# Kernel optimization log

Measured on AMD Instinct MI355X. Metric: run time of the kernel, lower is better.

Reference implementation:

```python
import jax, jax.numpy as jnp
import numpy as np

B, CIN, COUT, K, H, W = 16, 256, 256, 3, 64, 64
COND = 512


def setup_inputs() -> dict:
    key = jax.random.key(0)
    ks = jax.random.split(key, 10)
    X = jax.random.normal(ks[0], (B, CIN, H, W), dtype=jnp.float32)
    cond_v = jax.random.normal(ks[1], (B, COND), dtype=jnp.float32)
    # conv weight [O, I, kh, kw]
    conv_w = jax.random.normal(ks[2], (COUT, CIN, K, K), dtype=jnp.float32) / np.sqrt(CIN * K * K)
    w0 = jax.random.normal(ks[3], (COND, COND), dtype=jnp.float32) / np.sqrt(COND)
    b0 = jnp.zeros((COND,), dtype=jnp.float32)
    w1 = jax.random.normal(ks[4], (COND, COND), dtype=jnp.float32) / np.sqrt(COND)
    b1 = jnp.zeros((COND,), dtype=jnp.float32)
    w_out = jax.random.normal(ks[5], (CIN, COND), dtype=jnp.float32) / np.sqrt(COND)
    b_out = jnp.zeros((CIN,), dtype=jnp.float32)
    return {"X": X, "cond_v": cond_v, "conv_w": conv_w,
            "w0": w0, "b0": b0, "w1": w1, "b1": b1,
            "w_out": w_out, "b_out": b_out}


def reference(X, cond_v, conv_w, w0, b0, w1, b1, w_out, b_out):
    # proj_cond MLP: (Linear+SiLU) x depth, final Linear -> in_channels
    h = jax.nn.silu(cond_v @ w0.T + b0)
    h = jax.nn.silu(h @ w1.T + b1)
    scale = h @ w_out.T + b_out + 1.0          # [B, I]
    # modulate: bw[b,o,i,kh,kw] = w[o,i,kh,kw] * scale[b,i]
    bw = conv_w[None] * scale[:, None, :, None, None]
    # demodulate across (i, kh, kw)
    demod = jax.lax.rsqrt(jnp.sum(bw * bw, axis=(2, 3, 4)) + 1e-8)  # [B, O]
    bw = bw * demod[:, :, None, None, None]
    b, o, i, kh, kw = bw.shape
    # per-sample conv via grouped conv: x -> [1, B*I, H, W], w -> [B*O, I, kh, kw]
    x = X.reshape(1, b * i, X.shape[2], X.shape[3])
    w = bw.reshape(b * o, i, kh, kw)
    out = jax.lax.conv_general_dilated(
        x, w, window_strides=(1, 1), padding="SAME",
        feature_group_count=b,
        dimension_numbers=("NCHW", "OIHW", "NCHW"))
    return out.reshape(b, o, out.shape[2], out.shape[3])
```

## Files before the change

kernel.cpp:

```cpp
#include <hip/hip_runtime.h>
#include <hip/hip_bf16.h>
#include <cstdint>

#define NB 16
#define CI 256
#define CO 256
#define HH 64
#define WW 64
#define CC 512
#define HP 66
#define WP 66

typedef short short8 __attribute__((ext_vector_type(8)));
typedef float floatx4 __attribute__((ext_vector_type(4)));
typedef unsigned int uintx4 __attribute__((ext_vector_type(4)));

__device__ __forceinline__ void g2lds16(const void* g, void* l) {
  __builtin_amdgcn_global_load_lds((const __attribute__((address_space(1))) void*)g,
                                   (__attribute__((address_space(3))) void*)l, 16, 0, 0);
}

#define ASM_VMCNT0() do { __builtin_amdgcn_sched_barrier(0);               \
                          asm volatile("s_waitcnt vmcnt(0)" ::: "memory"); \
                          __builtin_amdgcn_sched_barrier(0); } while (0)
#define RAW_BAR() do { __builtin_amdgcn_sched_barrier(0);  \
                       __builtin_amdgcn_s_barrier();       \
                       __builtin_amdgcn_sched_barrier(0); } while (0)

__global__ __launch_bounds__(256)
void k_pre(const float* __restrict__ cw, __hip_bfloat16* __restrict__ Wt2,
           float* __restrict__ wsq,
           const float* __restrict__ cond_v, const float* __restrict__ w0,
           const float* __restrict__ b0, float* __restrict__ h0b) {
  int bid = blockIdx.x;
  if (bid < 256) {
    int gid = bid * 256 + threadIdx.x;
    int o = gid >> 8;
    int i = gid & 255;
    int base_i = ((i >> 5) * 4 + ((i >> 3) & 3)) * 2048 + o * 8 + (i & 7);
    const float* p = cw + (size_t)gid * 9;
    float s = 0.0f;
#pragma unroll
    for (int t = 0; t < 9; ++t) {
      float v = p[t];
      s += v * v;
      Wt2[(size_t)t * 65536 + base_i] = __float2bfloat16(v);
    }
    wsq[gid] = s;
  } else {
    __shared__ float4 sin4[CC / 4];
    int r = bid - 256;
    int b = r >> 1;
    int j = (r & 1) * 256 + threadIdx.x;
    const float4* in4 = reinterpret_cast<const float4*>(cond_v + (size_t)b * CC);
    if (threadIdx.x < CC / 4) sin4[threadIdx.x] = in4[threadIdx.x];
    __syncthreads();
    float a = b0[j];
    const float4* wr = reinterpret_cast<const float4*>(w0 + (size_t)j * CC);
#pragma unroll 8
    for (int kk = 0; kk < CC / 4; ++kk) {
      float4 w_ = wr[kk], v_ = sin4[kk];
      a += w_.x * v_.x + w_.y * v_.y + w_.z * v_.z + w_.w * v_.w;
    }
    a = a / (1.0f + __expf(-a));
    h0b[(size_t)b * CC + j] = a;
  }
}

template<int KD, int N, bool SILU, bool PLUSONE, int BJ>
__global__ void k_mlp(const float* __restrict__ in, const float* __restrict__ w,
                      const float* __restrict__ bias, float* __restrict__ out) {
  __shared__ float4 sin4[KD / 4];
  const int nb = N / BJ;
  int b = blockIdx.x / nb;
  int j = (blockIdx.x % nb) * BJ + threadIdx.x;
  const float4* in4 = reinterpret_cast<const float4*>(in + (size_t)b * KD);
  for (int k = threadIdx.x; k < KD / 4; k += BJ) sin4[k] = in4[k];
  __syncthreads();
  float acc = bias[j];
  const float4* wr = reinterpret_cast<const float4*>(w + (size_t)j * KD);
#pragma unroll 8
  for (int kk = 0; kk < KD / 4; ++kk) {
    float4 wv = wr[kk];
    float4 sv = sin4[kk];
    acc += wv.x * sv.x + wv.y * sv.y + wv.z * sv.z + wv.w * sv.w;
  }
  if (SILU) acc = acc / (1.0f + __expf(-acc));
  if (PLUSONE) acc += 1.0f;
  out[(size_t)b * N + j] = acc;
}

__global__ void k_scalex_demod(const float* __restrict__ X, const float* __restrict__ scale,
                               __hip_bfloat16* __restrict__ Xs,
                               const float* __restrict__ wsq, float* __restrict__ demod) {
  int bid = blockIdx.x;
  int t = threadIdx.x;
  if (bid >= NB * 256) {
    __shared__ float s2[CI];
    int b = bid - NB * 256;
    int o = t;
    float sv = scale[b * CI + o];
    s2[o] = sv * sv;
    __syncthreads();
    float acc = 0.0f;
    const float4* wr = reinterpret_cast<const float4*>(wsq + (size_t)o * CI);
    const float4* s4 = reinterpret_cast<const float4*>(s2);
#pragma unroll 8
    for (int i = 0; i < CI / 4; ++i) {
      float4 wv = wr[i], sq = s4[i];
      acc += wv.x * sq.x + wv.y * sq.y + wv.z * sq.z + wv.w * sq.w;
    }
    demod[(size_t)b * CO + o] = rsqrtf(acc + 1e-8f);
    return;
  }
  __shared__ float tile[64][68];
  __shared__ float ssc[64];
  int b = bid >> 8;
  int rem = bid & 255;
  int h = rem >> 2;
  int i0 = (rem & 3) * 64;
  if (t < 64) ssc[t] = scale[b * CI + i0 + t];

  __hip_bfloat16* xs_img = Xs + (size_t)b * HP * WP * CI;
  uintx4 z = {0u, 0u, 0u, 0u};
  if (t < 16) {
    int px = (t >> 3) * 65;
    int sl = t & 7;
    *reinterpret_cast<uintx4*>(xs_img + (((size_t)(h + 1)) * WP + px) * CI + i0 + sl * 8) = z;
  }
  if (h == 0) {
    for (int u = t; u < 66 * 8; u += 256) {
      int px = u >> 3, sl = u & 7;
      *reinterpret_cast<uintx4*>(xs_img + ((size_t)px) * CI + i0 + sl * 8) = z;
    }
  }
  if (h == 63) {
    for (int u = t; u < 66 * 8; u += 256) {
      int px = u >> 3, sl = u & 7;
      *reinterpret_cast<uintx4*>(xs_img + ((size_t)65 * WP + px) * CI + i0 + sl * 8) = z;
    }
  }

  const float* src = X + (((size_t)b * CI + i0) * HH + h) * WW;
  int ii_base = t >> 4;
  int w4 = (t & 15) * 4;
#pragma unroll
  for (int r2 = 0; r2 < 4; ++r2) {
    int ii = r2 * 16 + ii_base;
    int key = ((ii >> 3) & 7) << 2;
    *reinterpret_cast<float4*>(&tile[ii][w4 ^ key]) =
        *reinterpret_cast<const float4*>(src + (size_t)ii * HH * WW + w4);
  }
  __syncthreads();
  int u = t & 7;
  int wl = t >> 3;
  int key = u << 2;
#pragma unroll
  for (int iter = 0; iter < 2; ++iter) {
    int w2 = wl + iter * 32;
    union { unsigned short us[8]; uintx4 v; } pk;
#pragma unroll
    for (int j = 0; j < 8; ++j) {
      int ii = u * 8 + j;
      float v = tile[ii][w2 ^ key] * ssc[ii];
      __hip_bfloat16 hb = __float2bfloat16(v);
      pk.us[j] = *reinterpret_cast<unsigned short*>(&hb);
    }
    *reinterpret_cast<uintx4*>(xs_img + (((size_t)(h + 1)) * WP + (w2 + 1)) * CI + i0 + u * 8) = pk.v;
  }
}

__global__ __launch_bounds__(256, 2)
void k_conv(const __hip_bfloat16* __restrict__ Xs, const __hip_bfloat16* __restrict__ Wt2,
            const float* __restrict__ demod, float* __restrict__ out) {
  __shared__ __align__(16) char lds[2 * 28672];
  char* sX0 = lds;

  int wg = (blockIdx.x & 7) * 64 + (blockIdx.x >> 3);
  int b = wg >> 5;
  int rem = wg & 31;
  int ht = rem >> 1;
  int ob = rem & 1;
  int h0 = ht * 4;
  int o0 = ob * 128;

  int tid = threadIdx.x;
  int wv = tid >> 6;
  int lane = tid & 63;
  int lhi = lane >> 4;
  int llo = lane & 15;
  int wo2 = wv >> 1;
  int wpx = wv & 1;

  floatx4 acc[4][8];
#pragma unroll
  for (int m = 0; m < 4; ++m)
#pragma unroll
    for (int n = 0; n < 8; ++n) acc[m][n] = (floatx4){0.f, 0.f, 0.f, 0.f};

  const __hip_bfloat16* xs_img = Xs + (size_t)b * HP * WP * CI;

  int xoff[7];
#pragma unroll
  for (int s = 0; s < 7; ++s) {
    int j = wv + 4 * s;
    int pr = 16 * j + (lane >> 2);
    int prc = pr > 431 ? 431 : pr;
    int lr = prc / 72;
    int wp = prc - lr * 72;
    if (wp > 65) wp = 65;
    int ksl = (lane & 3) ^ ((pr >> 1) & 3);
    xoff[s] = ((h0 + lr) * WP + wp) * CI + ksl * 8;
  }
  int aofs[4];
#pragma unroll
  for (int m = 0; m < 4; ++m)
    aofs[m] = lhi * 2048 + (o0 + wo2 * 64 + m * 16 + llo) * 8;

#pragma unroll
  for (int s = 0; s < 7; ++s)
    g2lds16(xs_img + xoff[s], sX0 + (wv + 4 * s) * 1024);
  ASM_VMCNT0();
  RAW_BAR();

  for (int c = 0; c < 8; ++c) {
    const char* xbuf = sX0 + (c & 1) * 28672;
#pragma unroll
    for (int t = 0; t < 9; ++t) {
      const __hip_bfloat16* wb = Wt2 + (size_t)(t * 8 + c) * 8192;
      short8 af[4];
#pragma unroll
      for (int m = 0; m < 4; ++m)
        af[m] = *reinterpret_cast<const short8*>(wb + aofs[m]);
      if (t <= 6 && c < 7)
        g2lds16(xs_img + xoff[t] + (c + 1) * 32,
                sX0 + ((c + 1) & 1) * 28672 + (wv + 4 * t) * 1024);
      int kh = t / 3;
      int kw = t - kh * 3;
      __builtin_amdgcn_s_setprio(1);
#pragma unroll
      for (int n = 0; n < 8; ++n) {
        int stripe = wpx * 2 + (n >> 2) + kh;
        int px = (n & 3) * 16 + llo + kw;
        int prl = stripe * 72 + px;
        short8 bq = *reinterpret_cast<const short8*>(
            xbuf + prl * 64 + ((lhi ^ ((prl >> 1) & 3)) << 4));
#pragma unroll
        for (int m = 0; m < 4; ++m)
          acc[m][n] = __builtin_amdgcn_mfma_f32_16x16x32_bf16(af[m], bq, acc[m][n], 0, 0, 0);
      }
      __builtin_amdgcn_s_setprio(0);
      __builtin_amdgcn_sched_barrier(0);
    }
    ASM_VMCNT0();
    if (c < 7) RAW_BAR();
  }

#pragma unroll
  for (int m = 0; m < 4; ++m) {
    int obase_o = o0 + wo2 * 64 + m * 16 + lhi * 4;
    float4 dmv = *reinterpret_cast<const float4*>(demod + (size_t)b * CO + obase_o);
#pragma unroll
    for (int j = 0; j < 4; ++j) {
      int o = obase_o + j;
      float dm = (j == 0) ? dmv.x : (j == 1) ? dmv.y : (j == 2) ? dmv.z : dmv.w;
      float* orow = out + (((size_t)b * CO + o) * HH + h0) * WW;
#pragma unroll
      for (int n = 0; n < 8; ++n) {
        int row = wpx * 2 + (n >> 2);
        int col = (n & 3) * 16 + llo;
        orow[(size_t)row * WW + col] = acc[m][n][j] * dm;
      }
    }
  }
}

extern "C" void kernel_launch(void* const* d_in, const int* in_sizes, int n_in,
                              void* d_out, int out_size, void* d_ws, size_t ws_size,
                              hipStream_t stream) {
  const float* X      = (const float*)d_in[0];
  const float* cond_v = (const float*)d_in[1];
  const float* conv_w = (const float*)d_in[2];
  const float* w0     = (const float*)d_in[3];
  const float* b0     = (const float*)d_in[4];
  const float* w1     = (const float*)d_in[5];
  const float* b1     = (const float*)d_in[6];
  const float* w_out  = (const float*)d_in[7];
  const float* b_out  = (const float*)d_in[8];
  float* out = (float*)d_out;

  char* ws = (char*)d_ws;
  const size_t XS_BYTES  = (size_t)NB * HP * WP * CI * 2;
  const size_t WT_BYTES  = (size_t)9 * 65536 * 2;
  const size_t WSQ_BYTES = (size_t)CO * CI * 4;
  __hip_bfloat16* Xs  = (__hip_bfloat16*)ws;
  __hip_bfloat16* Wt2 = (__hip_bfloat16*)(ws + XS_BYTES);
  float* wsq   = (float*)(ws + XS_BYTES + WT_BYTES);
  float* h0b   = (float*)(ws + XS_BYTES + WT_BYTES + WSQ_BYTES);
  float* h1b   = h0b + NB * CC;
  float* scale = h1b + NB * CC;
  float* demod = scale + NB * CI;

  k_pre<<<288, 256, 0, stream>>>(conv_w, Wt2, wsq, cond_v, w0, b0, h0b);
  k_mlp<CC, CC, true, false, 128><<<NB * (CC / 128), 128, 0, stream>>>(h0b, w1, b1, h1b);
  k_mlp<CC, CI, false, true, 128><<<NB * (CI / 128), 128, 0, stream>>>(h1b, w_out, b_out, scale);
  k_scalex_demod<<<NB * 256 + NB, 256, 0, stream>>>(X, scale, Xs, wsq, demod);
  k_conv<<<NB * 32, 256, 0, stream>>>(Xs, Wt2, demod, out);
}
```

Measured before the change: 130.0 us.

## Halve conv output tile height to raise occupancy and grid size

New measurement: 149.3 us. 14.8% more time.

```diff
diff --git a/kernel.cpp b/kernel.cpp
--- a/kernel.cpp
+++ b/kernel.cpp
@@ -170,18 +170,18 @@
   }
 }
 
-__global__ __launch_bounds__(256, 2)
+__global__ __launch_bounds__(256, 3)
 void k_conv(const __hip_bfloat16* __restrict__ Xs, const __hip_bfloat16* __restrict__ Wt2,
             const float* __restrict__ demod, float* __restrict__ out) {
-  __shared__ __align__(16) char lds[2 * 28672];
+  __shared__ __align__(16) char lds[2 * 18432];
   char* sX0 = lds;
 
-  int wg = (blockIdx.x & 7) * 64 + (blockIdx.x >> 3);
-  int b = wg >> 5;
-  int rem = wg & 31;
+  int wg = (blockIdx.x & 7) * 128 + (blockIdx.x >> 3);
+  int b = wg >> 6;
+  int rem = wg & 63;
   int ht = rem >> 1;
   int ob = rem & 1;
-  int h0 = ht * 4;
+  int h0 = ht * 2;
   int o0 = ob * 128;
 
   int tid = threadIdx.x;
@@ -192,57 +192,59 @@
   int wo2 = wv >> 1;
   int wpx = wv & 1;
 
-  floatx4 acc[4][8];
+  floatx4 acc[4][4];
 #pragma unroll
   for (int m = 0; m < 4; ++m)
 #pragma unroll
-    for (int n = 0; n < 8; ++n) acc[m][n] = (floatx4){0.f, 0.f, 0.f, 0.f};
+    for (int n = 0; n < 4; ++n) acc[m][n] = (floatx4){0.f, 0.f, 0.f, 0.f};
 
   const __hip_bfloat16* xs_img = Xs + (size_t)b * HP * WP * CI;
 
-  int xoff[7];
-#pragma unroll
-  for (int s = 0; s < 7; ++s) {
+  int xoff[5];
+  const int nsl = (wv < 2) ? 5 : 4;
+#pragma unroll
+  for (int s = 0; s < 5; ++s) {
     int j = wv + 4 * s;
-    int pr = 16 * j + (lane >> 2);
-    int prc = pr > 431 ? 431 : pr;
-    int lr = prc / 72;
-    int wp = prc - lr * 72;
-    if (wp > 65) wp = 65;
-    int ksl = (lane & 3) ^ ((pr >> 1) & 3);
-    xoff[s] = ((h0 + lr) * WP + wp) * CI + ksl * 8;
-  }
-  int aofs[4];
-#pragma unroll
-  for (int m = 0; m < 4; ++m)
-    aofs[m] = lhi * 2048 + (o0 + wo2 * 64 + m * 16 + llo) * 8;
-
-#pragma unroll
-  for (int s = 0; s < 7; ++s)
-    g2lds16(xs_img + xoff[s], sX0 + (wv + 4 * s) * 1024);
+    if (j < 18) {
+      int pr = 16 * j + (lane >> 2);
+      int lr = pr / 72;
+      int wp = pr - lr * 72;
+      if (wp > 65) wp = 65;
+      int ksl = (lane & 3) ^ ((pr >> 1) & 3);
+      xoff[s] = ((h0 + lr) * WP + wp) * CI + ksl * 8;
+    } else {
+      xoff[s] = 0;
+    }
+  }
+  int abase = lhi * 2048 + (o0 + wo2 * 64 + llo) * 8;
+
+#pragma unroll
+  for (int s = 0; s < 5; ++s)
+    if (wv + 4 * s < 18)
+      g2lds16(xs_img + xoff[s], sX0 + (wv + 4 * s) * 1024);
   ASM_VMCNT0();
   RAW_BAR();
 
   for (int c = 0; c < 8; ++c) {
-    const char* xbuf = sX0 + (c & 1) * 28672;
+    const char* xbuf = sX0 + (c & 1) * 18432;
 #pragma unroll
     for (int t = 0; t < 9; ++t) {
-      const __hip_bfloat16* wb = Wt2 + (size_t)(t * 8 + c) * 8192;
+      const __hip_bfloat16* wb = Wt2 + (size_t)(t * 8 + c) * 8192 + abase;
       short8 af[4];
 #pragma unroll
       for (int m = 0; m < 4; ++m)
-        af[m] = *reinterpret_cast<const short8*>(wb + aofs[m]);
-      if (t <= 6 && c < 7)
-        g2lds16(xs_img + xoff[t] + (c + 1) * 32,
-                sX0 + ((c + 1) & 1) * 28672 + (wv + 4 * t) * 1024);
+        af[m] = *reinterpret_cast<const short8*>(wb + m * 128);
+      if (t < 5 && c < 7) {
+        if (t < nsl)
+          g2lds16(xs_img + xoff[t] + (c + 1) * 32,
+                  sX0 + ((c + 1) & 1) * 18432 + (wv + 4 * t) * 1024);
+      }
       int kh = t / 3;
       int kw = t - kh * 3;
       __builtin_amdgcn_s_setprio(1);
 #pragma unroll
-      for (int n = 0; n < 8; ++n) {
-        int stripe = wpx * 2 + (n >> 2) + kh;
-        int px = (n & 3) * 16 + llo + kw;
-        int prl = stripe * 72 + px;
+      for (int n = 0; n < 4; ++n) {
+        int prl = (wpx + kh) * 72 + n * 16 + llo + kw;
         short8 bq = *reinterpret_cast<const short8*>(
             xbuf + prl * 64 + ((lhi ^ ((prl >> 1) & 3)) << 4));
 #pragma unroll
@@ -264,13 +266,10 @@
     for (int j = 0; j < 4; ++j) {
       int o = obase_o + j;
       float dm = (j == 0) ? dmv.x : (j == 1) ? dmv.y : (j == 2) ? dmv.z : dmv.w;
-      float* orow = out + (((size_t)b * CO + o) * HH + h0) * WW;
-#pragma unroll
-      for (int n = 0; n < 8; ++n) {
-        int row = wpx * 2 + (n >> 2);
-        int col = (n & 3) * 16 + llo;
-        orow[(size_t)row * WW + col] = acc[m][n][j] * dm;
-      }
+      float* orow = out + (((size_t)b * CO + o) * HH + (h0 + wpx)) * WW;
+#pragma unroll
+      for (int n = 0; n < 4; ++n)
+        orow[n * 16 + llo] = acc[m][n][j] * dm;
     }
   }
 }
@@ -305,5 +304,5 @@
   k_mlp<CC, CC, true, false, 128><<<NB * (CC / 128), 128, 0, stream>>>(h0b, w1, b1, h1b);
   k_mlp<CC, CI, false, true, 128><<<NB * (CI / 128), 128, 0, stream>>>(h1b, w_out, b_out, scale);
   k_scalex_demod<<<NB * 256 + NB, 256, 0, stream>>>(X, scale, Xs, wsq, demod);
-  k_conv<<<NB * 32, 256, 0, stream>>>(Xs, Wt2, demod, out);
-}
+  k_conv<<<NB * 64, 256, 0, stream>>>(Xs, Wt2, demod, out);
+}
```
